# Kernel tuning notes

Hardware: AMD Instinct MI355X
Metric: run time of the kernel (lower is better)

Reference implementation:

```python
import jax, jax.numpy as jnp
import numpy as np

C, W, H = 16, 48, 48
OUTDIMS = 4000
COMPONENTS = 1
BATCH = 128
EPS = 1e-6
INIT_NOISE = 1e-3


def setup_inputs() -> dict:
    key = jax.random.key(0)
    kx, kw, kh, kf = jax.random.split(key, 4)
    x = jax.random.normal(kx, (BATCH, C, W, H), dtype=jnp.float32)
    width = jax.random.normal(kw, (OUTDIMS, 1, W, 1, COMPONENTS), dtype=jnp.float32) * INIT_NOISE
    height = jax.random.normal(kh, (OUTDIMS, 1, 1, H, COMPONENTS), dtype=jnp.float32) * INIT_NOISE
    features = jax.random.normal(kf, (OUTDIMS, C, 1, 1), dtype=jnp.float32) * INIT_NOISE
    bias = jnp.zeros((OUTDIMS,), dtype=jnp.float32)
    return {"x": x, "width": width, "height": height, "features": features, "bias": bias}


def reference(x, width, height, features, bias):
    # normalize width over the w axis (dim 2), height over the h axis (dim 3)
    wn = width / jnp.sqrt(jnp.sum(width * width, axis=2, keepdims=True) + EPS)
    hn = height / jnp.sqrt(jnp.sum(height * height, axis=3, keepdims=True) + EPS)
    # spatial mask: sum of outer products over components -> (outdims, w, h)
    spatial = jnp.sum(wn * hn, axis=4)[:, 0]  # broadcast (n,1,w,1,k)*(n,1,1,h,k)
    feat = features[:, :, 0, 0]  # (outdims, c)
    # y[b,n] = sum_{c,w,h} x[b,c,w,h] * spatial[n,w,h] * feat[n,c]  (same math as
    # x.view(N,-1) @ weight.t() where weight = spatial * features, flattened cwh)
    y = jnp.einsum('bcwh,nwh,nc->bn', x, spatial, feat)
    return y + bias[None, :]
```

## Files before the change

kernel.cpp:

```cpp
#include <hip/hip_runtime.h>
#include <stdint.h>

#define OUTD 4000
#define NPAD 4096
#define CC 16
#define WW 48
#define HH 48
#define BB 128
#define KD 768
#define MD 6144
#define EPSF 1e-6f

#define BM 384
#define BN 128
#define BKU 64
#define UNITS 12
#define AELEMS (BM * BKU)
#define SLOT_ELEMS ((BM + BN) * BKU)
#define THREADS 512
#define XPB 2304

using short8 = __attribute__((ext_vector_type(8))) short;
using f32x4  = __attribute__((ext_vector_type(4))) float;

static __device__ __forceinline__ unsigned short f2bf(float f) {
  union { float f; unsigned int u; } v; v.f = f;
  unsigned int u = v.u;
  unsigned int r = (u + 0x7FFFu + ((u >> 16) & 1u)) >> 16;
  return (unsigned short)r;
}

__global__ __launch_bounds__(256)
void prep_all(const float* __restrict__ x,
              const float* __restrict__ width,
              const float* __restrict__ height,
              const float* __restrict__ feat,
              unsigned short* __restrict__ A,
              unsigned short* __restrict__ Qt,
              float* __restrict__ wnT) {
  __shared__ float smw[4][WW];
  int bid = blockIdx.x;
  if (bid < XPB) {
    int t = bid * 256 + threadIdx.x;
    int e = t * 8;
    int h0 = e % HH;
    int w = (e / HH) % WW;
    int c = (e / (HH * WW)) % CC;
    int b = e / (HH * WW * CC);
    float4 v0 = *(const float4*)(x + e);
    float4 v1 = *(const float4*)(x + e + 4);
    short8 o;
    o[0] = (short)f2bf(v0.x); o[1] = (short)f2bf(v0.y);
    o[2] = (short)f2bf(v0.z); o[3] = (short)f2bf(v0.w);
    o[4] = (short)f2bf(v1.x); o[5] = (short)f2bf(v1.y);
    o[6] = (short)f2bf(v1.z); o[7] = (short)f2bf(v1.w);
    *(short8*)&A[(size_t)(b * WW + w) * KD + c * HH + h0] = o;
  } else {
    int lane = threadIdx.x & 63;
    int wv = threadIdx.x >> 6;
    int nbase = (bid - XPB) * 4;
    int n = nbase + wv;
    bool valid = (n < OUTD);
    float hv = (valid && lane < HH) ? height[n * HH + lane] : 0.f;
    float wvv = (valid && lane < WW) ? width[n * WW + lane] : 0.f;
    float hs = hv * hv, wsum = wvv * wvv;
    #pragma unroll
    for (int off = 32; off > 0; off >>= 1) {
      hs += __shfl_xor(hs, off);
      wsum += __shfl_xor(wsum, off);
    }
    float hnorm = rsqrtf(hs + EPSF);
    float wnorm = rsqrtf(wsum + EPSF);
    if (lane < WW) smw[wv][lane] = wvv * wnorm;
    if (valid) {
      #pragma unroll
      for (int i = lane; i < KD; i += 64) {
        int c = i / HH, h = i % HH;
        Qt[(size_t)n * KD + i] = f2bf(feat[n * CC + c] * height[n * HH + h] * hnorm);
      }
    } else {
      #pragma unroll
      for (int i = lane; i < KD; i += 64) Qt[(size_t)n * KD + i] = 0;
    }
    __syncthreads();
    if (threadIdx.x < WW) {
      int w = threadIdx.x;
      float4 o = make_float4(smw[0][w], smw[1][w], smw[2][w], smw[3][w]);
      *(float4*)&wnT[w * NPAD + nbase] = o;
    }
  }
}

__global__ __launch_bounds__(THREADS, 2)
void gemm_main(const unsigned short* __restrict__ A,
               const unsigned short* __restrict__ Qt,
               const float* __restrict__ wnT,
               const float* __restrict__ bias,
               float* __restrict__ out) {
  __shared__ unsigned short S[2 * SLOT_ELEMS];

  int tid = threadIdx.x;
  int lane = tid & 63;
  int wid = tid >> 6;
  int wm = wid >> 1;
  int wnh = wid & 1;

  int bid = blockIdx.x;
  int xcd = bid & 7;
  int i = bid >> 3;
  int by = xcd * 2 + (i & 1);
  int bx = i >> 1;
  int n0 = bx * BN;
  int m0 = by * BM;

  int rsub = lane >> 3;
  int cg = lane & 7;
  int gsw = (cg ^ rsub) * 8;
  const unsigned short* gA[6];
  const unsigned short* gB[2];
  #pragma unroll
  for (int j = 0; j < 6; ++j)
    gA[j] = A + (size_t)(m0 + (wid * 6 + j) * 8 + rsub) * KD + gsw;
  #pragma unroll
  for (int j = 0; j < 2; ++j)
    gB[j] = Qt + (size_t)(n0 + (wid * 2 + j) * 8 + rsub) * KD + gsw;
  int aD[6], bD[2];
  #pragma unroll
  for (int j = 0; j < 6; ++j) aD[j] = (wid * 6 + j) * 512;
  #pragma unroll
  for (int j = 0; j < 2; ++j) bD[j] = AELEMS + (wid * 2 + j) * 512;

#define SLOTB(u) (((u) & 1) * SLOT_ELEMS)
#define STAGE(u)                                                                    \
  { _Pragma("unroll")                                                               \
    for (int j = 0; j < 6; ++j)                                                     \
      __builtin_amdgcn_global_load_lds(                                             \
          (const __attribute__((address_space(1))) void*)(gA[j] + (u) * BKU),       \
          (__attribute__((address_space(3))) void*)(&S[SLOTB(u) + aD[j]]), 16, 0, 0); \
    _Pragma("unroll")                                                               \
    for (int j = 0; j < 2; ++j)                                                     \
      __builtin_amdgcn_global_load_lds(                                             \
          (const __attribute__((address_space(1))) void*)(gB[j] + (u) * BKU),       \
          (__attribute__((address_space(3))) void*)(&S[SLOTB(u) + bD[j]]), 16, 0, 0); }

  int q16 = lane & 15;
  int hi = lane >> 4;
  int q7 = q16 & 7;
  int aofs[2], bofs[2];
  #pragma unroll
  for (int kh = 0; kh < 2; ++kh) {
    aofs[kh] = (wm * 96 + q16) * BKU + (((kh * 4 + hi) ^ q7) * 8);
    bofs[kh] = AELEMS + (wnh * 64 + q16) * BKU + (((kh * 4 + hi) ^ q7) * 8);
  }

  f32x4 acc[6][4] = {};
  short8 afA[6], bfA[4], afB[6], bfB[4];

#define DSREAD_H(afX, bfX, u, kh)                                      \
  { const unsigned short* sb = &S[SLOTB(u)];                           \
    _Pragma("unroll")                                                  \
    for (int mi = 0; mi < 6; ++mi)                                     \
      afX[mi] = *(const short8*)&sb[aofs[kh] + mi * 16 * BKU];         \
    _Pragma("unroll")                                                  \
    for (int ni = 0; ni < 4; ++ni)                                     \
      bfX[ni] = *(const short8*)&sb[bofs[kh] + ni * 16 * BKU]; }

#define MFMA24(afX, bfX)                                               \
  { _Pragma("unroll")                                                  \
    for (int ni = 0; ni < 4; ++ni)                                     \
      _Pragma("unroll")                                                \
      for (int mi = 0; mi < 6; ++mi)                                   \
        acc[mi][ni] = __builtin_amdgcn_mfma_f32_16x16x32_bf16(afX[mi], bfX[ni], acc[mi][ni], 0, 0, 0); }

  STAGE(0);

  #pragma unroll
  for (int u = 0; u < UNITS; ++u) {
    if (u + 1 < UNITS) STAGE(u + 1);
    if (u + 1 < UNITS) asm volatile("s_waitcnt vmcnt(8)" ::: "memory");
    else               asm volatile("s_waitcnt vmcnt(0)" ::: "memory");
    __builtin_amdgcn_s_barrier();
    __builtin_amdgcn_sched_barrier(0);

    DSREAD_H(afA, bfA, u, 0);
    asm volatile("s_waitcnt lgkmcnt(0)" ::: "memory");
    __builtin_amdgcn_sched_barrier(0);
    DSREAD_H(afB, bfB, u, 1);
    __builtin_amdgcn_s_setprio(1);
    MFMA24(afA, bfA);
    asm volatile("s_waitcnt lgkmcnt(0)" ::: "memory");
    __builtin_amdgcn_sched_barrier(0);
    MFMA24(afB, bfB);
    __builtin_amdgcn_s_setprio(0);
    __builtin_amdgcn_sched_barrier(0);
  }

  int b0 = by * 8 + wm * 2;
  #pragma unroll
  for (int ni = 0; ni < 4; ++ni) {
    int ng = n0 + wnh * 64 + ni * 16 + q16;
    float s0 = 0.f, s1 = 0.f;
    #pragma unroll
    for (int mi = 0; mi < 3; ++mi) {
      int wbase = mi * 16 + hi * 4;
      f32x4 va = acc[mi][ni];
      f32x4 vb = acc[mi + 3][ni];
      #pragma unroll
      for (int r = 0; r < 4; ++r) {
        float t = wnT[(wbase + r) * NPAD + ng];
        s0 += t * va[r];
        s1 += t * vb[r];
      }
    }
    s0 += __shfl_xor(s0, 16); s0 += __shfl_xor(s0, 32);
    s1 += __shfl_xor(s1, 16); s1 += __shfl_xor(s1, 32);
    if (hi == 0 && ng < OUTD) {
      float bv = bias[ng];
      out[(size_t)b0 * OUTD + ng] = s0 + bv;
      out[(size_t)(b0 + 1) * OUTD + ng] = s1 + bv;
    }
  }
#undef STAGE
#undef SLOTB
#undef DSREAD_H
#undef MFMA24
}

extern "C" void kernel_launch(void* const* d_in, const int* in_sizes, int n_in,
                              void* d_out, int out_size, void* d_ws, size_t ws_size,
                              hipStream_t stream) {
  const float* x      = (const float*)d_in[0];
  const float* width  = (const float*)d_in[1];
  const float* height = (const float*)d_in[2];
  const float* feat   = (const float*)d_in[3];
  const float* bias   = (const float*)d_in[4];
  float* out = (float*)d_out;

  char* ws = (char*)d_ws;
  unsigned short* A  = (unsigned short*)ws;
  unsigned short* Qt = (unsigned short*)(ws + 9437184);
  float* wnT         = (float*)(ws + 9437184 + 6291456);

  prep_all<<<dim3(XPB + NPAD / 4), dim3(256), 0, stream>>>(x, width, height, feat, A, Qt, wnT);
  gemm_main<<<dim3(512), dim3(THREADS), 0, stream>>>(A, Qt, wnT, bias, out);
}
```

Before: 49.88 us.

## Load B operand fragments directly from global into registers, bypassing LDS

```diff
diff --git a/kernel.cpp b/kernel.cpp
--- a/kernel.cpp
+++ b/kernel.cpp
@@ -15,8 +15,7 @@
 #define BN 128
 #define BKU 64
 #define UNITS 12
-#define AELEMS (BM * BKU)
-#define SLOT_ELEMS ((BM + BN) * BKU)
+#define SLOT_ELEMS (BM * BKU)
 #define THREADS 512
 #define XPB 2304
 
@@ -117,80 +116,83 @@
   int cg = lane & 7;
   int gsw = (cg ^ rsub) * 8;
   const unsigned short* gA[6];
-  const unsigned short* gB[2];
   #pragma unroll
   for (int j = 0; j < 6; ++j)
     gA[j] = A + (size_t)(m0 + (wid * 6 + j) * 8 + rsub) * KD + gsw;
-  #pragma unroll
-  for (int j = 0; j < 2; ++j)
-    gB[j] = Qt + (size_t)(n0 + (wid * 2 + j) * 8 + rsub) * KD + gsw;
-  int aD[6], bD[2];
+  int aD[6];
   #pragma unroll
   for (int j = 0; j < 6; ++j) aD[j] = (wid * 6 + j) * 512;
-  #pragma unroll
-  for (int j = 0; j < 2; ++j) bD[j] = AELEMS + (wid * 2 + j) * 512;
 
 #define SLOTB(u) (((u) & 1) * SLOT_ELEMS)
-#define STAGE(u)                                                                    \
+#define STAGE_A(u)                                                                  \
   { _Pragma("unroll")                                                               \
     for (int j = 0; j < 6; ++j)                                                     \
       __builtin_amdgcn_global_load_lds(                                             \
           (const __attribute__((address_space(1))) void*)(gA[j] + (u) * BKU),       \
-          (__attribute__((address_space(3))) void*)(&S[SLOTB(u) + aD[j]]), 16, 0, 0); \
-    _Pragma("unroll")                                                               \
-    for (int j = 0; j < 2; ++j)                                                     \
-      __builtin_amdgcn_global_load_lds(                                             \
-          (const __attribute__((address_space(1))) void*)(gB[j] + (u) * BKU),       \
-          (__attribute__((address_space(3))) void*)(&S[SLOTB(u) + bD[j]]), 16, 0, 0); }
+          (__attribute__((address_space(3))) void*)(&S[SLOTB(u) + aD[j]]), 16, 0, 0); }
 
   int q16 = lane & 15;
   int hi = lane >> 4;
+  const unsigned short* gQ[4];
+  #pragma unroll
+  for (int ni = 0; ni < 4; ++ni)
+    gQ[ni] = Qt + (size_t)(n0 + wnh * 64 + ni * 16 + q16) * KD + hi * 8;
+
+  short8 bfr[2][8];
+#define BLOAD(set, u)                                                   \
+  { _Pragma("unroll")                                                   \
+    for (int kh = 0; kh < 2; ++kh)                                      \
+      _Pragma("unroll")                                                 \
+      for (int ni = 0; ni < 4; ++ni)                                    \
+        bfr[set][kh * 4 + ni] = *(const short8*)&gQ[ni][(u) * BKU + kh * 32]; }
+
   int q7 = q16 & 7;
-  int aofs[2], bofs[2];
-  #pragma unroll
-  for (int kh = 0; kh < 2; ++kh) {
+  int aofs[2];
+  #pragma unroll
+  for (int kh = 0; kh < 2; ++kh)
     aofs[kh] = (wm * 96 + q16) * BKU + (((kh * 4 + hi) ^ q7) * 8);
-    bofs[kh] = AELEMS + (wnh * 64 + q16) * BKU + (((kh * 4 + hi) ^ q7) * 8);
-  }
 
   f32x4 acc[6][4] = {};
-  short8 afA[6], bfA[4], afB[6], bfB[4];
-
-#define DSREAD_H(afX, bfX, u, kh)                                      \
+  short8 afA[6], afB[6];
+
+#define DSREAD_A(afX, u, kh)                                           \
   { const unsigned short* sb = &S[SLOTB(u)];                           \
     _Pragma("unroll")                                                  \
     for (int mi = 0; mi < 6; ++mi)                                     \
-      afX[mi] = *(const short8*)&sb[aofs[kh] + mi * 16 * BKU];         \
-    _Pragma("unroll")                                                  \
-    for (int ni = 0; ni < 4; ++ni)                                     \
-      bfX[ni] = *(const short8*)&sb[bofs[kh] + ni * 16 * BKU]; }
-
-#define MFMA24(afX, bfX)                                               \
+      afX[mi] = *(const short8*)&sb[aofs[kh] + mi * 16 * BKU]; }
+
+#define MFMA24(afX, kh, cs)                                            \
   { _Pragma("unroll")                                                  \
     for (int ni = 0; ni < 4; ++ni)                                     \
       _Pragma("unroll")                                                \
       for (int mi = 0; mi < 6; ++mi)                                   \
-        acc[mi][ni] = __builtin_amdgcn_mfma_f32_16x16x32_bf16(afX[mi], bfX[ni], acc[mi][ni], 0, 0, 0); }
-
-  STAGE(0);
+        acc[mi][ni] = __builtin_amdgcn_mfma_f32_16x16x32_bf16(afX[mi], bfr[cs][(kh) * 4 + ni], acc[mi][ni], 0, 0, 0); }
+
+  STAGE_A(0);
+  BLOAD(0, 0);
 
   #pragma unroll
   for (int u = 0; u < UNITS; ++u) {
-    if (u + 1 < UNITS) STAGE(u + 1);
-    if (u + 1 < UNITS) asm volatile("s_waitcnt vmcnt(8)" ::: "memory");
-    else               asm volatile("s_waitcnt vmcnt(0)" ::: "memory");
+    const int cs = u & 1;
+    if (u + 1 < UNITS) {
+      STAGE_A(u + 1);
+      BLOAD(cs ^ 1, u + 1);
+      asm volatile("s_waitcnt vmcnt(14)" ::: "memory");
+    } else {
+      asm volatile("s_waitcnt vmcnt(0)" ::: "memory");
+    }
     __builtin_amdgcn_s_barrier();
     __builtin_amdgcn_sched_barrier(0);
 
-    DSREAD_H(afA, bfA, u, 0);
+    DSREAD_A(afA, u, 0);
     asm volatile("s_waitcnt lgkmcnt(0)" ::: "memory");
     __builtin_amdgcn_sched_barrier(0);
-    DSREAD_H(afB, bfB, u, 1);
+    DSREAD_A(afB, u, 1);
     __builtin_amdgcn_s_setprio(1);
-    MFMA24(afA, bfA);
+    MFMA24(afA, 0, cs);
     asm volatile("s_waitcnt lgkmcnt(0)" ::: "memory");
     __builtin_amdgcn_sched_barrier(0);
-    MFMA24(afB, bfB);
+    MFMA24(afB, 1, cs);
     __builtin_amdgcn_s_setprio(0);
     __builtin_amdgcn_sched_barrier(0);
   }
@@ -220,9 +222,10 @@
       out[(size_t)(b0 + 1) * OUTD + ng] = s1 + bv;
     }
   }
-#undef STAGE
+#undef STAGE_A
 #undef SLOTB
-#undef DSREAD_H
+#undef BLOAD
+#undef DSREAD_A
 #undef MFMA24
 }
 
```

Result: slower. 75.18 us (+50.7%).

## Widen GEMM N-tile to 256 with split A/B LDS buffers and interleaved reads

Applied to the files above, without the earlier changes.

```diff
diff --git a/kernel.cpp b/kernel.cpp
--- a/kernel.cpp
+++ b/kernel.cpp
@@ -12,11 +12,11 @@
 #define EPSF 1e-6f
 
 #define BM 384
-#define BN 128
+#define BNB 256
 #define BKU 64
 #define UNITS 12
 #define AELEMS (BM * BKU)
-#define SLOT_ELEMS ((BM + BN) * BKU)
+#define BELEMS (BNB * BKU)
 #define THREADS 512
 #define XPB 2304
 
@@ -97,7 +97,7 @@
                const float* __restrict__ wnT,
                const float* __restrict__ bias,
                float* __restrict__ out) {
-  __shared__ unsigned short S[2 * SLOT_ELEMS];
+  __shared__ unsigned short S[2 * AELEMS + 2 * BELEMS];
 
   int tid = threadIdx.x;
   int lane = tid & 63;
@@ -109,121 +109,144 @@
   int xcd = bid & 7;
   int i = bid >> 3;
   int by = xcd * 2 + (i & 1);
-  int bx = i >> 1;
-  int n0 = bx * BN;
+  int bxg = i >> 1;
+  int n0 = bxg * BNB;
   int m0 = by * BM;
 
   int rsub = lane >> 3;
   int cg = lane & 7;
   int gsw = (cg ^ rsub) * 8;
   const unsigned short* gA[6];
-  const unsigned short* gB[2];
+  const unsigned short* gB[4];
   #pragma unroll
   for (int j = 0; j < 6; ++j)
     gA[j] = A + (size_t)(m0 + (wid * 6 + j) * 8 + rsub) * KD + gsw;
   #pragma unroll
-  for (int j = 0; j < 2; ++j)
-    gB[j] = Qt + (size_t)(n0 + (wid * 2 + j) * 8 + rsub) * KD + gsw;
-  int aD[6], bD[2];
-  #pragma unroll
-  for (int j = 0; j < 6; ++j) aD[j] = (wid * 6 + j) * 512;
-  #pragma unroll
-  for (int j = 0; j < 2; ++j) bD[j] = AELEMS + (wid * 2 + j) * 512;
-
-#define SLOTB(u) (((u) & 1) * SLOT_ELEMS)
+  for (int j = 0; j < 4; ++j)
+    gB[j] = Qt + (size_t)(n0 + (wid * 4 + j) * 8 + rsub) * KD + gsw;
+
+#define ASLOT(u) (((u) & 1) * AELEMS)
+#define BSLOT(u) (2 * AELEMS + ((u) & 1) * BELEMS)
 #define STAGE(u)                                                                    \
   { _Pragma("unroll")                                                               \
     for (int j = 0; j < 6; ++j)                                                     \
       __builtin_amdgcn_global_load_lds(                                             \
           (const __attribute__((address_space(1))) void*)(gA[j] + (u) * BKU),       \
-          (__attribute__((address_space(3))) void*)(&S[SLOTB(u) + aD[j]]), 16, 0, 0); \
+          (__attribute__((address_space(3))) void*)(&S[ASLOT(u) + (wid * 6 + j) * 512]), 16, 0, 0); \
     _Pragma("unroll")                                                               \
-    for (int j = 0; j < 2; ++j)                                                     \
+    for (int j = 0; j < 4; ++j)                                                     \
       __builtin_amdgcn_global_load_lds(                                             \
           (const __attribute__((address_space(1))) void*)(gB[j] + (u) * BKU),       \
-          (__attribute__((address_space(3))) void*)(&S[SLOTB(u) + bD[j]]), 16, 0, 0); }
+          (__attribute__((address_space(3))) void*)(&S[BSLOT(u) + (wid * 4 + j) * 512]), 16, 0, 0); }
 
   int q16 = lane & 15;
   int hi = lane >> 4;
   int q7 = q16 & 7;
-  int aofs[2], bofs[2];
-  #pragma unroll
-  for (int kh = 0; kh < 2; ++kh) {
-    aofs[kh] = (wm * 96 + q16) * BKU + (((kh * 4 + hi) ^ q7) * 8);
-    bofs[kh] = AELEMS + (wnh * 64 + q16) * BKU + (((kh * 4 + hi) ^ q7) * 8);
-  }
-
-  f32x4 acc[6][4] = {};
-  short8 afA[6], bfA[4], afB[6], bfB[4];
-
-#define DSREAD_H(afX, bfX, u, kh)                                      \
-  { const unsigned short* sb = &S[SLOTB(u)];                           \
-    _Pragma("unroll")                                                  \
-    for (int mi = 0; mi < 6; ++mi)                                     \
-      afX[mi] = *(const short8*)&sb[aofs[kh] + mi * 16 * BKU];         \
-    _Pragma("unroll")                                                  \
-    for (int ni = 0; ni < 4; ++ni)                                     \
-      bfX[ni] = *(const short8*)&sb[bofs[kh] + ni * 16 * BKU]; }
-
-#define MFMA24(afX, bfX)                                               \
-  { _Pragma("unroll")                                                  \
-    for (int ni = 0; ni < 4; ++ni)                                     \
-      _Pragma("unroll")                                                \
-      for (int mi = 0; mi < 6; ++mi)                                   \
-        acc[mi][ni] = __builtin_amdgcn_mfma_f32_16x16x32_bf16(afX[mi], bfX[ni], acc[mi][ni], 0, 0, 0); }
+  int kg[2];
+  kg[0] = ((0 * 4 + hi) ^ q7) * 8;
+  kg[1] = ((1 * 4 + hi) ^ q7) * 8;
+  int arow = (wm * 96 + q16) * BKU;
+  int brow = (wnh * 32 + q16) * BKU;
+
+  f32x4 acc[8][6] = {};
+  short8 af[6];
+  short8 bf0[2], bf1[2];
+
+#define READ_AF(u, kh)                                                  \
+  { const unsigned short* sb = &S[ASLOT(u) + arow + kg[kh]];            \
+    _Pragma("unroll")                                                   \
+    for (int mi = 0; mi < 6; ++mi)                                      \
+      af[mi] = *(const short8*)&sb[mi * 16 * BKU]; }
+
+#define READ_BF(dst, u, bx, kh)                                         \
+  { const unsigned short* sb = &S[BSLOT(u) + brow + (bx) * 64 * BKU + kg[kh]]; \
+    dst[0] = *(const short8*)&sb[0];                                    \
+    dst[1] = *(const short8*)&sb[16 * BKU]; }
+
+#define MFMA12(bfs, bx)                                                 \
+  { __builtin_amdgcn_s_setprio(1);                                      \
+    _Pragma("unroll")                                                   \
+    for (int ni2 = 0; ni2 < 2; ++ni2)                                   \
+      _Pragma("unroll")                                                 \
+      for (int mi = 0; mi < 6; ++mi)                                    \
+        acc[(bx) * 2 + ni2][mi] = __builtin_amdgcn_mfma_f32_16x16x32_bf16(af[mi], bfs[ni2], acc[(bx) * 2 + ni2][mi], 0, 0, 0); \
+    __builtin_amdgcn_s_setprio(0); }
+
+#define LGKM(n) { asm volatile("s_waitcnt lgkmcnt(" #n ")" ::: "memory"); __builtin_amdgcn_sched_barrier(0); }
 
   STAGE(0);
 
   #pragma unroll
   for (int u = 0; u < UNITS; ++u) {
-    if (u + 1 < UNITS) STAGE(u + 1);
-    if (u + 1 < UNITS) asm volatile("s_waitcnt vmcnt(8)" ::: "memory");
-    else               asm volatile("s_waitcnt vmcnt(0)" ::: "memory");
+    asm volatile("s_waitcnt vmcnt(0)" ::: "memory");
     __builtin_amdgcn_s_barrier();
     __builtin_amdgcn_sched_barrier(0);
-
-    DSREAD_H(afA, bfA, u, 0);
-    asm volatile("s_waitcnt lgkmcnt(0)" ::: "memory");
-    __builtin_amdgcn_sched_barrier(0);
-    DSREAD_H(afB, bfB, u, 1);
-    __builtin_amdgcn_s_setprio(1);
-    MFMA24(afA, bfA);
-    asm volatile("s_waitcnt lgkmcnt(0)" ::: "memory");
-    __builtin_amdgcn_sched_barrier(0);
-    MFMA24(afB, bfB);
-    __builtin_amdgcn_s_setprio(0);
+    if (u + 1 < UNITS) STAGE(u + 1);
+
+    READ_AF(u, 0);
+    READ_BF(bf0, u, 0, 0);
+    LGKM(0);
+    READ_BF(bf1, u, 1, 0);
+    MFMA12(bf0, 0);
+    READ_BF(bf0, u, 2, 0);
+    LGKM(2);
+    MFMA12(bf1, 1);
+    READ_BF(bf1, u, 3, 0);
+    LGKM(2);
+    MFMA12(bf0, 2);
+    LGKM(0);
+    MFMA12(bf1, 3);
+    READ_AF(u, 1);
+    READ_BF(bf0, u, 0, 1);
+    LGKM(0);
+    READ_BF(bf1, u, 1, 1);
+    MFMA12(bf0, 0);
+    READ_BF(bf0, u, 2, 1);
+    LGKM(2);
+    MFMA12(bf1, 1);
+    READ_BF(bf1, u, 3, 1);
+    LGKM(2);
+    MFMA12(bf0, 2);
+    LGKM(0);
+    MFMA12(bf1, 3);
     __builtin_amdgcn_sched_barrier(0);
   }
 
   int b0 = by * 8 + wm * 2;
   #pragma unroll
-  for (int ni = 0; ni < 4; ++ni) {
-    int ng = n0 + wnh * 64 + ni * 16 + q16;
-    float s0 = 0.f, s1 = 0.f;
+  for (int bx = 0; bx < 4; ++bx) {
     #pragma unroll
-    for (int mi = 0; mi < 3; ++mi) {
-      int wbase = mi * 16 + hi * 4;
-      f32x4 va = acc[mi][ni];
-      f32x4 vb = acc[mi + 3][ni];
+    for (int ni2 = 0; ni2 < 2; ++ni2) {
+      int ng = n0 + bx * 64 + wnh * 32 + ni2 * 16 + q16;
+      float s0 = 0.f, s1 = 0.f;
       #pragma unroll
-      for (int r = 0; r < 4; ++r) {
-        float t = wnT[(wbase + r) * NPAD + ng];
-        s0 += t * va[r];
-        s1 += t * vb[r];
+      for (int mi = 0; mi < 3; ++mi) {
+        int wbase = mi * 16 + hi * 4;
+        f32x4 va = acc[bx * 2 + ni2][mi];
+        f32x4 vb = acc[bx * 2 + ni2][mi + 3];
+        #pragma unroll
+        for (int r = 0; r < 4; ++r) {
+          float t = wnT[(wbase + r) * NPAD + ng];
+          s0 += t * va[r];
+          s1 += t * vb[r];
+        }
       }
-    }
-    s0 += __shfl_xor(s0, 16); s0 += __shfl_xor(s0, 32);
-    s1 += __shfl_xor(s1, 16); s1 += __shfl_xor(s1, 32);
-    if (hi == 0 && ng < OUTD) {
-      float bv = bias[ng];
-      out[(size_t)b0 * OUTD + ng] = s0 + bv;
-      out[(size_t)(b0 + 1) * OUTD + ng] = s1 + bv;
+      s0 += __shfl_xor(s0, 16); s0 += __shfl_xor(s0, 32);
+      s1 += __shfl_xor(s1, 16); s1 += __shfl_xor(s1, 32);
+      if (hi == 0 && ng < OUTD) {
+        float bv = bias[ng];
+        out[(size_t)b0 * OUTD + ng] = s0 + bv;
+        out[(size_t)(b0 + 1) * OUTD + ng] = s1 + bv;
+      }
     }
   }
 #undef STAGE
-#undef SLOTB
-#undef DSREAD_H
-#undef MFMA24
+#undef ASLOT
+#undef BSLOT
+#undef READ_AF
+#undef READ_BF
+#undef MFMA12
+#undef LGKM
 }
 
 extern "C" void kernel_launch(void* const* d_in, const int* in_sizes, int n_in,
@@ -242,5 +265,5 @@
   float* wnT         = (float*)(ws + 9437184 + 6291456);
 
   prep_all<<<dim3(XPB + NPAD / 4), dim3(256), 0, stream>>>(x, width, height, feat, A, Qt, wnT);
-  gemm_main<<<dim3(512), dim3(THREADS), 0, stream>>>(A, Qt, wnT, bias, out);
-}
+  gemm_main<<<dim3(256), dim3(THREADS), 0, stream>>>(A, Qt, wnT, bias, out);
+}
```

Measured after the change: 80.35 us. 61.1% more time.
